# Performance work log

Measured on AMD Instinct MI355X. Metric: run time of the kernel, lower is better.

## Reference

```python
import jax, jax.numpy as jnp
import numpy as np


def _log_g(x):
    # log_g(x) = log(relu(x)+1) if x >= 0 else x
    return jnp.where(x >= 0, jnp.log1p(jnp.maximum(x, 0.0)), x)


def _min_gru(hg):
    # hg: [B, H, L] -> [B, H/2, L]
    h, gate = jnp.split(hg, 2, axis=1)
    log_coeffs = -jax.nn.softplus(gate)                    # log(1 - z)
    log_values = -jax.nn.softplus(-gate) + _log_g(h)       # log(z) + log g(h)
    a_star = jnp.cumsum(log_coeffs, axis=2)
    log_h0_plus_b_star = jax.lax.cumlogsumexp(log_values - a_star, axis=2)
    return jnp.exp(a_star + log_h0_plus_b_star)


def setup_inputs() -> dict:
    key = jax.random.key(0)
    B, H, L = 8, 512, 8192
    x = jax.random.normal(key, (B, H, L), dtype=jnp.float32)
    return {"x": x}


def reference(x) -> jnp.ndarray:
    # bidirectional minGRU: forward scan on first half of channels,
    # reversed scan on second half.
    fore, back = jnp.split(x, 2, axis=1)
    out_fore = _min_gru(fore)
    out_back = jnp.flip(_min_gru(jnp.flip(back, axis=2)), axis=2)
    return jnp.concatenate([out_fore, out_back], axis=1)  # [B, H/2, L]
```

## Files before the change

kernel.cpp:

```cpp
#include <hip/hip_runtime.h>
#include <math.h>


#define SEQ_L 8192
#define NTHREADS 256
#define PER_THREAD 8
#define TILE (NTHREADS * PER_THREAD)
#define NTILES (SEQ_L / TILE)

__global__ __launch_bounds__(NTHREADS) void mingru_scan_kernel(
    const float* __restrict__ x, float* __restrict__ out) {
    const int blk = blockIdx.x;
    const int dir = blk >> 10;
    const int s   = blk & 1023;
    const int b   = s >> 7;
    const int c   = s & 127;

    const int tid  = threadIdx.x;
    const int lane = tid & 63;
    const int wave = tid >> 6;

    const float* __restrict__ hrow = x + (size_t)((b * 512) + (dir * 256) + c) * SEQ_L;
    const float* __restrict__ grow = hrow + (size_t)128 * SEQ_L;
    float* __restrict__ orow = out + (size_t)((b * 256) + (dir * 128) + c) * SEQ_L;

    __shared__ float sA[2][4];
    __shared__ float sB[2][4];

    float carry = 0.0f;

    {
    }
    int base0 = tid * PER_THREAD;
    int idx0  = dir ? (SEQ_L - base0 - PER_THREAD) : base0;
    float4 nh0 = *(const float4*)(hrow + idx0);
    float4 nh1 = *(const float4*)(hrow + idx0 + 4);
    float4 ng0 = *(const float4*)(grow + idx0);
    float4 ng1 = *(const float4*)(grow + idx0 + 4);

#pragma unroll
    for (int t = 0; t < NTILES; ++t) {
        const float4 h0 = nh0, h1 = nh1, g0 = ng0, g1 = ng1;

        if (t + 1 < NTILES) {
            const int nb = (t + 1) * TILE + tid * PER_THREAD;
            const int ni = dir ? (SEQ_L - nb - PER_THREAD) : nb;
            nh0 = *(const float4*)(hrow + ni);
            nh1 = *(const float4*)(hrow + ni + 4);
            ng0 = *(const float4*)(grow + ni);
            ng1 = *(const float4*)(grow + ni + 4);
        }

        float hv[PER_THREAD], gv[PER_THREAD];
        if (dir == 0) {
            hv[0]=h0.x; hv[1]=h0.y; hv[2]=h0.z; hv[3]=h0.w;
            hv[4]=h1.x; hv[5]=h1.y; hv[6]=h1.z; hv[7]=h1.w;
            gv[0]=g0.x; gv[1]=g0.y; gv[2]=g0.z; gv[3]=g0.w;
            gv[4]=g1.x; gv[5]=g1.y; gv[6]=g1.z; gv[7]=g1.w;
        } else {
            hv[0]=h1.w; hv[1]=h1.z; hv[2]=h1.y; hv[3]=h1.x;
            hv[4]=h0.w; hv[5]=h0.z; hv[6]=h0.y; hv[7]=h0.x;
            gv[0]=g1.w; gv[1]=g1.z; gv[2]=g1.y; gv[3]=g1.x;
            gv[4]=g0.w; gv[5]=g0.z; gv[6]=g0.y; gv[7]=g0.x;
        }

        float pp[PER_THREAD], ov0[PER_THREAD];
        float ca = 1.0f, cb = 0.0f;
#pragma unroll
        for (int j = 0; j < PER_THREAD; ++j) {
            const float gt = gv[j];
            const float e  = __expf(-fabsf(gt));
            const float r  = 1.0f / (1.0f + e);
            const float sn = e * r;
            const float z  = (gt >= 0.0f) ? r  : sn;
            const float a  = (gt >= 0.0f) ? sn : r;
            const float hh = hv[j];
            const float gf = (hh >= 0.0f) ? (hh + 1.0f) : __expf(hh);
            const float bb = z * gf;
            cb = a * cb + bb;
            ca = a * ca;
            ov0[j] = cb;
            pp[j]  = ca;
        }

        float pa = ca, pb = cb;
#pragma unroll
        for (int d = 1; d < 64; d <<= 1) {
            const float oa = __shfl_up(pa, d);
            const float ob = __shfl_up(pb, d);
            if (lane >= d) {
                pb = pa * ob + pb;
                pa = pa * oa;
            }
        }

        const int buf = t & 1;
        if (lane == 63) { sA[buf][wave] = pa; sB[buf][wave] = pb; }
        __syncthreads();

        float st = carry;
        for (int w = 0; w < wave; ++w) st = sA[buf][w] * st + sB[buf][w];
        float ea = __shfl_up(pa, 1);
        float eb = __shfl_up(pb, 1);
        if (lane == 0) { ea = 1.0f; eb = 0.0f; }
        st = ea * st + eb;

        float ov[PER_THREAD];
#pragma unroll
        for (int j = 0; j < PER_THREAD; ++j) ov[j] = ov0[j] + st * pp[j];

        const int base = t * TILE + tid * PER_THREAD;
        if (dir == 0) {
            *(float4*)(orow + base)     = make_float4(ov[0], ov[1], ov[2], ov[3]);
            *(float4*)(orow + base + 4) = make_float4(ov[4], ov[5], ov[6], ov[7]);
        } else {
            const int p = SEQ_L - base - PER_THREAD;
            *(float4*)(orow + p)     = make_float4(ov[7], ov[6], ov[5], ov[4]);
            *(float4*)(orow + p + 4) = make_float4(ov[3], ov[2], ov[1], ov[0]);
        }

        float nc = carry;
#pragma unroll
        for (int w = 0; w < 4; ++w) nc = sA[buf][w] * nc + sB[buf][w];
        carry = nc;
    }
}

extern "C" void kernel_launch(void* const* d_in, const int* in_sizes, int n_in,
                              void* d_out, int out_size, void* d_ws, size_t ws_size,
                              hipStream_t stream) {
    const float* x = (const float*)d_in[0];
    float* out = (float*)d_out;
    mingru_scan_kernel<<<2048, NTHREADS, 0, stream>>>(x, out);
}
```

Before: 209.6 us.

## Use single-wave blocks with register prefetch queue, removing LDS and barriers

Each channel row is now scanned by one 64-lane wave that walks 16 sub-tiles of 512 elements in sequence, carrying the running state with a lane-63 broadcast. This removes the cross-wave shared-memory combine and the __syncthreads per tile. To hide memory latency, a four-deep register queue prefetches upcoming sub-tiles. The cost is only 2048 single-wave blocks, so there is far less parallelism per row and a longer serial chain, plus higher register pressure from the queue.

```diff
diff --git a/kernel.cpp b/kernel.cpp
--- a/kernel.cpp
+++ b/kernel.cpp
@@ -3,55 +3,54 @@
 
 
 #define SEQ_L 8192
-#define NTHREADS 256
-#define PER_THREAD 8
-#define TILE (NTHREADS * PER_THREAD)
-#define NTILES (SEQ_L / TILE)
+#define PER_LANE 8
+#define SUB (64 * PER_LANE)
+#define NSUB (SEQ_L / SUB)
+#define DQ 4
 
-__global__ __launch_bounds__(NTHREADS) void mingru_scan_kernel(
+__global__ __launch_bounds__(64, 2) void mingru_scan_kernel(
     const float* __restrict__ x, float* __restrict__ out) {
     const int blk = blockIdx.x;
     const int dir = blk >> 10;
     const int s   = blk & 1023;
     const int b   = s >> 7;
     const int c   = s & 127;
-
-    const int tid  = threadIdx.x;
-    const int lane = tid & 63;
-    const int wave = tid >> 6;
+    const int lane = threadIdx.x;
 
     const float* __restrict__ hrow = x + (size_t)((b * 512) + (dir * 256) + c) * SEQ_L;
     const float* __restrict__ grow = hrow + (size_t)128 * SEQ_L;
     float* __restrict__ orow = out + (size_t)((b * 256) + (dir * 128) + c) * SEQ_L;
 
-    __shared__ float sA[2][4];
-    __shared__ float sB[2][4];
+    float4 qh0[DQ], qh1[DQ], qg0[DQ], qg1[DQ];
+
+#pragma unroll
+    for (int k = 0; k < DQ; ++k) {
+        const int base = k * SUB + lane * PER_LANE;
+        const int p = dir ? (SEQ_L - base - PER_LANE) : base;
+        qh0[k] = *(const float4*)(hrow + p);
+        qh1[k] = *(const float4*)(hrow + p + 4);
+        qg0[k] = *(const float4*)(grow + p);
+        qg1[k] = *(const float4*)(grow + p + 4);
+    }
 
     float carry = 0.0f;
 
-    {
-    }
-    int base0 = tid * PER_THREAD;
-    int idx0  = dir ? (SEQ_L - base0 - PER_THREAD) : base0;
-    float4 nh0 = *(const float4*)(hrow + idx0);
-    float4 nh1 = *(const float4*)(hrow + idx0 + 4);
-    float4 ng0 = *(const float4*)(grow + idx0);
-    float4 ng1 = *(const float4*)(grow + idx0 + 4);
+#pragma unroll
+    for (int t = 0; t < NSUB; ++t) {
+        const int slot = t & (DQ - 1);
+        const float4 h0 = qh0[slot], h1 = qh1[slot];
+        const float4 g0 = qg0[slot], g1 = qg1[slot];
 
-#pragma unroll
-    for (int t = 0; t < NTILES; ++t) {
-        const float4 h0 = nh0, h1 = nh1, g0 = ng0, g1 = ng1;
-
-        if (t + 1 < NTILES) {
-            const int nb = (t + 1) * TILE + tid * PER_THREAD;
-            const int ni = dir ? (SEQ_L - nb - PER_THREAD) : nb;
-            nh0 = *(const float4*)(hrow + ni);
-            nh1 = *(const float4*)(hrow + ni + 4);
-            ng0 = *(const float4*)(grow + ni);
-            ng1 = *(const float4*)(grow + ni + 4);
+        if (t + DQ < NSUB) {
+            const int nb = (t + DQ) * SUB + lane * PER_LANE;
+            const int np = dir ? (SEQ_L - nb - PER_LANE) : nb;
+            qh0[slot] = *(const float4*)(hrow + np);
+            qh1[slot] = *(const float4*)(hrow + np + 4);
+            qg0[slot] = *(const float4*)(grow + np);
+            qg1[slot] = *(const float4*)(grow + np + 4);
         }
 
-        float hv[PER_THREAD], gv[PER_THREAD];
+        float hv[PER_LANE], gv[PER_LANE];
         if (dir == 0) {
             hv[0]=h0.x; hv[1]=h0.y; hv[2]=h0.z; hv[3]=h0.w;
             hv[4]=h1.x; hv[5]=h1.y; hv[6]=h1.z; hv[7]=h1.w;
@@ -64,10 +63,10 @@
             gv[4]=g0.w; gv[5]=g0.z; gv[6]=g0.y; gv[7]=g0.x;
         }
 
-        float pp[PER_THREAD], ov0[PER_THREAD];
+        float pp[PER_LANE], ov0[PER_LANE];
         float ca = 1.0f, cb = 0.0f;
 #pragma unroll
-        for (int j = 0; j < PER_THREAD; ++j) {
+        for (int j = 0; j < PER_LANE; ++j) {
             const float gt = gv[j];
             const float e  = __expf(-fabsf(gt));
             const float r  = 1.0f / (1.0f + e);
@@ -94,35 +93,28 @@
             }
         }
 
-        const int buf = t & 1;
-        if (lane == 63) { sA[buf][wave] = pa; sB[buf][wave] = pb; }
-        __syncthreads();
-
-        float st = carry;
-        for (int w = 0; w < wave; ++w) st = sA[buf][w] * st + sB[buf][w];
         float ea = __shfl_up(pa, 1);
         float eb = __shfl_up(pb, 1);
         if (lane == 0) { ea = 1.0f; eb = 0.0f; }
-        st = ea * st + eb;
+        const float st = ea * carry + eb;
 
-        float ov[PER_THREAD];
+        float ov[PER_LANE];
 #pragma unroll
-        for (int j = 0; j < PER_THREAD; ++j) ov[j] = ov0[j] + st * pp[j];
+        for (int j = 0; j < PER_LANE; ++j) ov[j] = ov0[j] + st * pp[j];
 
-        const int base = t * TILE + tid * PER_THREAD;
+        const int base = t * SUB + lane * PER_LANE;
         if (dir == 0) {
             *(float4*)(orow + base)     = make_float4(ov[0], ov[1], ov[2], ov[3]);
             *(float4*)(orow + base + 4) = make_float4(ov[4], ov[5], ov[6], ov[7]);
         } else {
-            const int p = SEQ_L - base - PER_THREAD;
+            const int p = SEQ_L - base - PER_LANE;
             *(float4*)(orow + p)     = make_float4(ov[7], ov[6], ov[5], ov[4]);
             *(float4*)(orow + p + 4) = make_float4(ov[3], ov[2], ov[1], ov[0]);
         }
 
-        float nc = carry;
-#pragma unroll
-        for (int w = 0; w < 4; ++w) nc = sA[buf][w] * nc + sB[buf][w];
-        carry = nc;
+        const float ga = __shfl(pa, 63);
+        const float gb = __shfl(pb, 63);
+        carry = ga * carry + gb;
     }
 }
 
@@ -131,5 +123,5 @@
                               hipStream_t stream) {
     const float* x = (const float*)d_in[0];
     float* out = (float*)d_out;
-    mingru_scan_kernel<<<2048, NTHREADS, 0, stream>>>(x, out);
+    mingru_scan_kernel<<<2048, 64, 0, stream>>>(x, out);
 }
```

Result: slower. 218.3 us (+4.2%).
